# Performance work log

Measured on AMD Instinct MI355X. Metric: run time of the kernel, lower is better.

## Reference

```python
import jax, jax.numpy as jnp
import numpy as np

EPS = 1e-8  # torch cosine_similarity default eps


def setup_inputs() -> dict:
    key = jax.random.key(0)
    k1, k2, k3 = jax.random.split(key, 3)
    B, N, D = 16, 4096, 256
    embeddings_stat = jax.random.normal(k1, (B, N, D), dtype=jnp.float32)
    embeddings_con = jax.random.normal(k2, (B, N, D), dtype=jnp.float32)
    # ragged row counts per instance (0 allowed -> instance skipped, as in source)
    lengths = jax.random.randint(k3, (B,), 0, 4096)
    return {
        "embeddings_stat": embeddings_stat,
        "embeddings_con": embeddings_con,
        "lengths": lengths,
    }


def reference(embeddings_stat, embeddings_con, lengths):
    # embeddings_stat, embeddings_con: [B, N, D]; lengths: [B] valid row counts
    B, N, D = embeddings_stat.shape
    dt = embeddings_stat.dtype
    mask = (jnp.arange(N)[None, :] < lengths[:, None]).astype(dt)  # [B, N]

    dot = jnp.sum(embeddings_stat * embeddings_con, axis=-1)        # [B, N]
    n_stat = jnp.maximum(jnp.sqrt(jnp.sum(embeddings_stat**2, -1)), EPS)
    n_con = jnp.maximum(jnp.sqrt(jnp.sum(embeddings_con**2, -1)), EPS)
    cos = dot / (n_stat * n_con)                                    # [B, N]

    denom = jnp.maximum(lengths, 1).astype(dt)                      # avoid /0
    mean_cos = jnp.sum(cos * mask, axis=-1) / denom                 # [B]
    per_inst = jnp.where(lengths > 0, 1.0 - mean_cos, 0.0)          # skip empty
    mean_cosine_loss = jnp.sum(per_inst) / B
    return mean_cosine_loss[None]  # shape [1], matching torch output
```

## Files before the change

kernel.cpp:

```cpp
#include <hip/hip_runtime.h>

#define NROWS 4096
#define DDIM 256
#define BLOCKS_PER_B 64

__global__ __launch_bounds__(256) void cos_partial_kernel(
    const float* __restrict__ stat, const float* __restrict__ con,
    const int* __restrict__ lens, float* __restrict__ ws) {
  const int blk  = blockIdx.x;
  const int b    = blk / BLOCKS_PER_B;
  const int j    = blk % BLOCKS_PER_B;
  const int wave = threadIdx.x >> 6;
  const int lane = threadIdx.x & 63;

  const int len = lens[b];

  float acc = 0.0f;
  for (int n = j + (wave << 6); n < len; n += 256) {
    const size_t base = ((size_t)b * NROWS + (size_t)n) * DDIM + (size_t)(lane << 2);
    const float4 a = *reinterpret_cast<const float4*>(stat + base);
    const float4 c = *reinterpret_cast<const float4*>(con + base);

    float dot = a.x * c.x + a.y * c.y + a.z * c.z + a.w * c.w;
    float ns  = a.x * a.x + a.y * a.y + a.z * a.z + a.w * a.w;
    float nc  = c.x * c.x + c.y * c.y + c.z * c.z + c.w * c.w;

    #pragma unroll
    for (int off = 32; off > 0; off >>= 1) {
      dot += __shfl_xor(dot, off);
      ns  += __shfl_xor(ns,  off);
      nc  += __shfl_xor(nc,  off);
    }
    const float denom = fmaxf(sqrtf(ns), 1e-8f) * fmaxf(sqrtf(nc), 1e-8f);
    acc += dot / denom;
  }

  __shared__ float sh[4];
  if (lane == 0) sh[wave] = acc;
  __syncthreads();
  if (threadIdx.x == 0) ws[blk] = sh[0] + sh[1] + sh[2] + sh[3];
}

__global__ __launch_bounds__(1024) void cos_final_kernel(
    const float* __restrict__ ws, const int* __restrict__ lens,
    float* __restrict__ out, int B) {
  const int w    = threadIdx.x >> 6;
  const int lane = threadIdx.x & 63;

  float v = 0.0f;
  if (w < B) v = ws[w * BLOCKS_PER_B + lane];
  #pragma unroll
  for (int off = 32; off > 0; off >>= 1) v += __shfl_xor(v, off);

  __shared__ float sh[16];
  if (lane == 0 && w < B) {
    const int len = lens[w];
    sh[w] = (len > 0) ? (1.0f - v / (float)len) : 0.0f;
  }
  __syncthreads();
  if (threadIdx.x == 0) {
    float t = 0.0f;
    for (int i = 0; i < B; ++i) t += sh[i];
    out[0] = t / (float)B;
  }
}

extern "C" void kernel_launch(void* const* d_in, const int* in_sizes, int n_in,
                              void* d_out, int out_size, void* d_ws, size_t ws_size,
                              hipStream_t stream) {
  const float* stat = (const float*)d_in[0];
  const float* con  = (const float*)d_in[1];
  const int*   lens = (const int*)d_in[2];
  float*       out  = (float*)d_out;
  float*       ws   = (float*)d_ws;

  const int B = in_sizes[2];

  dim3 grid1(B * BLOCKS_PER_B);
  dim3 blk1(256);
  hipLaunchKernelGGL(cos_partial_kernel, grid1, blk1, 0, stream, stat, con, lens, ws);

  dim3 grid2(1);
  dim3 blk2(64 * B);
  hipLaunchKernelGGL(cos_final_kernel, grid2, blk2, 0, stream, ws, lens, out, B);
}
```

Measured before the change: 22.64 us.

## Map one wave per row index across all batches for ragged load balance

Work is redistributed so each wave handles a fixed row index n and loops over all 16 batch instances. Before, each batch had its own set of blocks, and the cost of those blocks depended on that batch's length. Spreading rows across 1024 blocks evens out the ragged lengths across CUs and puts 16 independent loads in flight per wave. The cost is a larger workspace, a longer final reduction (1024 partials per batch), and B hardcoded to 16.

```diff
diff --git a/kernel.cpp b/kernel.cpp
--- a/kernel.cpp
+++ b/kernel.cpp
@@ -2,60 +2,78 @@
 
 #define NROWS 4096
 #define DDIM 256
-#define BLOCKS_PER_B 64
+#define BDIM 16
+#define NBLOCKS 1024
 
 __global__ __launch_bounds__(256) void cos_partial_kernel(
     const float* __restrict__ stat, const float* __restrict__ con,
     const int* __restrict__ lens, float* __restrict__ ws) {
-  const int blk  = blockIdx.x;
-  const int b    = blk / BLOCKS_PER_B;
-  const int j    = blk % BLOCKS_PER_B;
-  const int wave = threadIdx.x >> 6;
+  const int widx = threadIdx.x >> 6;
   const int lane = threadIdx.x & 63;
+  const int w    = (blockIdx.x << 2) + widx;
+  const int n    = w;
 
-  const int len = lens[b];
+  int L[BDIM];
+  #pragma unroll
+  for (int b = 0; b < BDIM; ++b) L[b] = lens[b];
 
-  float acc = 0.0f;
-  for (int n = j + (wave << 6); n < len; n += 256) {
-    const size_t base = ((size_t)b * NROWS + (size_t)n) * DDIM + (size_t)(lane << 2);
-    const float4 a = *reinterpret_cast<const float4*>(stat + base);
-    const float4 c = *reinterpret_cast<const float4*>(con + base);
+  float acc[BDIM];
+  #pragma unroll
+  for (int b = 0; b < BDIM; ++b) acc[b] = 0.0f;
 
-    float dot = a.x * c.x + a.y * c.y + a.z * c.z + a.w * c.w;
-    float ns  = a.x * a.x + a.y * a.y + a.z * a.z + a.w * a.w;
-    float nc  = c.x * c.x + c.y * c.y + c.z * c.z + c.w * c.w;
+  #pragma unroll
+  for (int b = 0; b < BDIM; ++b) {
+    if (n < L[b]) {
+      const size_t base = ((size_t)b * NROWS + (size_t)n) * DDIM + (size_t)(lane << 2);
+      const float4 a = *reinterpret_cast<const float4*>(stat + base);
+      const float4 c = *reinterpret_cast<const float4*>(con + base);
 
-    #pragma unroll
-    for (int off = 32; off > 0; off >>= 1) {
-      dot += __shfl_xor(dot, off);
-      ns  += __shfl_xor(ns,  off);
-      nc  += __shfl_xor(nc,  off);
+      float dot = a.x * c.x + a.y * c.y + a.z * c.z + a.w * c.w;
+      float ns  = a.x * a.x + a.y * a.y + a.z * a.z + a.w * a.w;
+      float nc  = c.x * c.x + c.y * c.y + c.z * c.z + c.w * c.w;
+
+      #pragma unroll
+      for (int off = 32; off > 0; off >>= 1) {
+        dot += __shfl_xor(dot, off);
+        ns  += __shfl_xor(ns,  off);
+        nc  += __shfl_xor(nc,  off);
+      }
+      const float denom = fmaxf(sqrtf(ns), 1e-8f) * fmaxf(sqrtf(nc), 1e-8f);
+      acc[b] = dot / denom;
     }
-    const float denom = fmaxf(sqrtf(ns), 1e-8f) * fmaxf(sqrtf(nc), 1e-8f);
-    acc += dot / denom;
   }
 
-  __shared__ float sh[4];
-  if (lane == 0) sh[wave] = acc;
+  __shared__ float sh[4][BDIM];
+  if (lane == 0) {
+    #pragma unroll
+    for (int b = 0; b < BDIM; ++b) sh[widx][b] = acc[b];
+  }
   __syncthreads();
-  if (threadIdx.x == 0) ws[blk] = sh[0] + sh[1] + sh[2] + sh[3];
+  const int t = threadIdx.x;
+  if (t < BDIM) {
+    ws[t * NBLOCKS + blockIdx.x] = sh[0][t] + sh[1][t] + sh[2][t] + sh[3][t];
+  }
 }
 
 __global__ __launch_bounds__(1024) void cos_final_kernel(
     const float* __restrict__ ws, const int* __restrict__ lens,
     float* __restrict__ out, int B) {
-  const int w    = threadIdx.x >> 6;
+  const int b    = threadIdx.x >> 6;
   const int lane = threadIdx.x & 63;
 
   float v = 0.0f;
-  if (w < B) v = ws[w * BLOCKS_PER_B + lane];
+  if (b < B) {
+    #pragma unroll
+    for (int m = 0; m < NBLOCKS / 64; ++m)
+      v += ws[b * NBLOCKS + lane + (m << 6)];
+  }
   #pragma unroll
   for (int off = 32; off > 0; off >>= 1) v += __shfl_xor(v, off);
 
-  __shared__ float sh[16];
-  if (lane == 0 && w < B) {
-    const int len = lens[w];
-    sh[w] = (len > 0) ? (1.0f - v / (float)len) : 0.0f;
+  __shared__ float sh[BDIM];
+  if (lane == 0 && b < B) {
+    const int len = lens[b];
+    sh[b] = (len > 0) ? (1.0f - v / (float)len) : 0.0f;
   }
   __syncthreads();
   if (threadIdx.x == 0) {
@@ -76,11 +94,11 @@
 
   const int B = in_sizes[2];
 
-  dim3 grid1(B * BLOCKS_PER_B);
+  dim3 grid1(NBLOCKS);
   dim3 blk1(256);
   hipLaunchKernelGGL(cos_partial_kernel, grid1, blk1, 0, stream, stat, con, lens, ws);
 
   dim3 grid2(1);
-  dim3 blk2(64 * B);
+  dim3 blk2(64 * BDIM);
   hipLaunchKernelGGL(cos_final_kernel, grid2, blk2, 0, stream, ws, lens, out, B);
 }
```

Result: faster. 21.59 us (-4.7%).
